# Kernel optimization log

Hardware: AMD Instinct MI355X
Metric: run time of the kernel (lower is better)

Reference implementation:

```python
import jax, jax.numpy as jnp
import numpy as np

B, S = 4, 1024
D = 256          # token_dim = channel_dim = expert_dim
D_LF = 768       # longformer hidden size
ADAPT = 128
NEXP = 4
HID = 64
DSUM = 3 * D + D_LF  # combiner concat width = 1536


def _gelu(v):
    return jax.nn.gelu(v, approximate=False)  # torch nn.GELU default = exact


def setup_inputs() -> dict:
    key = jax.random.key(0)
    ks = iter(jax.random.split(key, 40))
    def w(shape, scale=1.0):
        return jax.random.normal(next(ks), shape, jnp.float32) * scale
    z = lambda *shape: jnp.zeros(shape, jnp.float32)
    return dict(
        x=w((B, S, D)),
        lf_out=w((B, S, D_LF)),
        W_feat=w((D, ADAPT), D ** -0.5), b_feat=z(ADAPT),
        Wt=w((D, D), D ** -0.5), bt=z(D),
        Wt_a=w((ADAPT, D * D), 0.01 * ADAPT ** -0.5), bt_a=z(D * D),
        Wc=w((D, D), D ** -0.5), bc=z(D),
        Wc_a=w((ADAPT, D * D), 0.01 * ADAPT ** -0.5), bc_a=z(D * D),
        We=w((NEXP, D, D), D ** -0.5), be=z(NEXP, D),
        We_a=w((NEXP, ADAPT, D * D), 0.01 * ADAPT ** -0.5), be_a=z(NEXP, D * D),
        Wg=w((ADAPT, NEXP + 1), ADAPT ** -0.5), bg=z(NEXP + 1),
        Wphi=w((D, HID)), bphi=z(D, HID),
        Wpsi1=w((D * HID, HID), (D * HID) ** -0.5), bpsi1=z(HID),
        Wpsi2=w((HID, D), HID ** -0.5), bpsi2=z(D),
        Wres=w((DSUM, DSUM), DSUM ** -0.5), bres=z(DSUM),
        W1=w((DSUM, HID), DSUM ** -0.5), b1=z(HID),
        W2=w((HID, 4), HID ** -0.5), b2=z(4),
        Wo=w((DSUM, D), DSUM ** -0.5), bo=z(D),
    )


def reference(x, lf_out, W_feat, b_feat, Wt, bt, Wt_a, bt_a, Wc, bc, Wc_a, bc_a,
              We, be, We_a, be_a, Wg, bg, Wphi, bphi, Wpsi1, bpsi1, Wpsi2, bpsi2,
              Wres, bres, W1, b1, W2, b2, Wo, bo):
    Bx, Sx, d = x.shape
    N = Bx * Sx
    xf = x.reshape(N, d)
    lff = lf_out.reshape(N, -1)
    # featurizer -> per-token adapt features; global mean drives adaptive weights
    adapt = xf @ W_feat + b_feat            # [N, ADAPT]
    am = adapt.mean(axis=0)                 # [ADAPT] single adapt vector (LiquidLinear view constraint)

    def liquid(inp, Wb, bb, Wa, ba):
        Wdyn = Wb + (am @ Wa + ba).reshape(Wb.shape)
        return inp @ Wdyn + bb

    tok = liquid(xf, Wt, bt, Wt_a, bt_a)    # [N, D] token mixer
    chan = liquid(xf, Wc, bc, Wc_a, bc_a)   # [N, D] channel mixer

    # MixtureOfExperts: softmax gate over NEXP liquid experts + 1 KA expert
    gate = jax.nn.softmax(adapt @ Wg + bg, axis=-1)              # [N, NEXP+1]
    dW = (jnp.einsum('a,eaf->ef', am, We_a) + be_a).reshape(We.shape)
    eo = jnp.einsum('nd,edo->neo', xf, We + dW) + be[None]       # [N, E, D]
    # Kolmogorov-Arnold expert: per-feature phi (Linear(1,HID)+gelu), then psi MLP
    phi = _gelu(xf[:, :, None] * Wphi[None] + bphi[None])        # [N, D, HID]
    ka = _gelu(phi.reshape(N, -1) @ Wpsi1 + bpsi1) @ Wpsi2 + bpsi2
    moe = jnp.einsum('ne,ned->nd', gate[:, :-1], eo) + gate[:, -1:] * ka

    # ComponentCombination: learned softmax component weights + residual path
    concat = jnp.concatenate([tok, chan, moe, lff], axis=-1)     # [N, DSUM]
    residual = concat @ Wres + bres
    h = _gelu(concat @ W1 + b1)
    cw = jax.nn.softmax(h @ W2 + b2, axis=-1)                    # [N, 4]
    combined = jnp.concatenate(
        [cw[:, 0:1] * tok, cw[:, 1:2] * chan, cw[:, 2:3] * moe, cw[:, 3:4] * lff],
        axis=-1) + residual                                      # [N, DSUM]
    return (combined @ Wo + bo).reshape(Bx, Sx, d)
```

## Files before the change

### kernel.cpp

```cpp
#include <hip/hip_runtime.h>
#include <hip/hip_bf16.h>


__device__ __forceinline__ float gelu_f(float v){ return 0.5f*v*(1.0f + erff(v*0.70710678118654752f)); }

__device__ __forceinline__ float u16tof(unsigned short u){
  union { unsigned int i; float f; } v; v.i = ((unsigned int)u) << 16; return v.f;
}
__device__ __forceinline__ unsigned short f2b(float f){
  union { float f; unsigned int u; } v; v.f = f;
  unsigned int r = v.u + 0x7fffu + ((v.u >> 16) & 1u);
  return (unsigned short)(r >> 16);
}

using short8  = __attribute__((ext_vector_type(8))) short;
using float4v = __attribute__((ext_vector_type(4))) float;

template<int MODE>
__global__ __launch_bounds__(256) void mgemm_k(
    const unsigned short* __restrict__ A, const unsigned short* __restrict__ Bt,
    const float* __restrict__ bias, float* __restrict__ C,
    int M, int N, int K, long sB, long sBias, long sC)
{
  if constexpr (MODE==1){
    Bt   += sB   * blockIdx.z;
    bias += sBias* blockIdx.z;
    C    += sC   * blockIdx.z;
  }
  __shared__ __align__(16) unsigned short As[128][40];
  __shared__ __align__(16) unsigned short Bs[128][40];
  const int tid  = threadIdx.x;
  const int m0   = blockIdx.y*128, n0 = blockIdx.x*128;
  const int wave = tid>>6, lane = tid&63;
  const int wm   = (wave&1)*64, wn = (wave>>1)*64;
  const int q    = lane>>4, r = lane&15;
  const int sm   = tid>>2, sq = (tid&3)*8;

  float4v acc[4][4];
  #pragma unroll
  for (int i=0;i<4;i++)
    #pragma unroll
    for (int j=0;j<4;j++) acc[i][j] = (float4v){0.f,0.f,0.f,0.f};

  const unsigned short* Ap = A + (long)(m0+sm)*K + sq;
  const unsigned short* Bp = Bt + (long)(n0+sm)*K + sq;
  const long rstep = (long)64*K;

  for (int k0 = 0; k0 < K; k0 += 32){
    uint4 a0 = *(const uint4*)(Ap + k0);
    uint4 a1 = *(const uint4*)(Ap + k0 + rstep);
    uint4 b0 = *(const uint4*)(Bp + k0);
    uint4 b1 = *(const uint4*)(Bp + k0 + rstep);
    __syncthreads();
    *(uint4*)&As[sm   ][sq] = a0;
    *(uint4*)&As[sm+64][sq] = a1;
    *(uint4*)&Bs[sm   ][sq] = b0;
    *(uint4*)&Bs[sm+64][sq] = b1;
    __syncthreads();
    short8 af[4], bf[4];
    #pragma unroll
    for (int mt=0;mt<4;mt++) af[mt] = *(const short8*)&As[wm + mt*16 + r][q*8];
    #pragma unroll
    for (int nt=0;nt<4;nt++) bf[nt] = *(const short8*)&Bs[wn + nt*16 + r][q*8];
    #pragma unroll
    for (int mt=0;mt<4;mt++)
      #pragma unroll
      for (int nt=0;nt<4;nt++)
        acc[mt][nt] = __builtin_amdgcn_mfma_f32_16x16x32_bf16(af[mt], bf[nt], acc[mt][nt], 0, 0, 0);
  }

  #pragma unroll
  for (int nt=0;nt<4;nt++){
    int col = n0 + wn + nt*16 + r;
    float bb = bias[col];
    #pragma unroll
    for (int mt=0;mt<4;mt++){
      #pragma unroll
      for (int i=0;i<4;i++){
        int row = m0 + wm + mt*16 + q*4 + i;
        C[(long)row*N + col] = acc[mt][nt][i] + bb;
      }
    }
  }
}

__global__ __launch_bounds__(256) void psi1m_k(const float* __restrict__ x,
    const float* __restrict__ Wphi, const float* __restrict__ bphi,
    const unsigned short* __restrict__ Wpsi1_t, float* __restrict__ h1)
{
  __shared__ float xs[64][33];
  __shared__ __align__(16) unsigned int wbls[32][64];
  __shared__ __align__(16) unsigned short As[64][72];
  __shared__ __align__(16) unsigned short Bs[64][72];
  const int tid = threadIdx.x;
  const int m0 = blockIdx.x*64, d_lo = blockIdx.y*32;

  {
    int m = tid>>2, off = (tid&3)*8;
    const float* src = x + (long)(m0+m)*256 + d_lo + off;
    #pragma unroll
    for (int i=0;i<8;i++) xs[m][off+i] = src[i];
  }
  {
    #pragma unroll
    for (int i=0;i<2;i++){
      int idx4 = tid + 256*i;
      int rr = idx4>>4, cc = (idx4&15)*4;
      float4 w4 = *(const float4*)&Wphi[(long)(d_lo+rr)*64 + cc];
      float4 b4 = *(const float4*)&bphi[(long)(d_lo+rr)*64 + cc];
      uint4 p;
      p.x = (unsigned int)f2b(w4.x) | ((unsigned int)f2b(b4.x)<<16);
      p.y = (unsigned int)f2b(w4.y) | ((unsigned int)f2b(b4.y)<<16);
      p.z = (unsigned int)f2b(w4.z) | ((unsigned int)f2b(b4.z)<<16);
      p.w = (unsigned int)f2b(w4.w) | ((unsigned int)f2b(b4.w)<<16);
      *(uint4*)&wbls[rr][cc] = p;
    }
  }
  const int wave = tid>>6, lane = tid&63;
  const int wm = (wave&1)*32, wn = (wave>>1)*32;
  const int q = lane>>4, r = lane&15;
  const int pm = tid>>2, pk = (tid&3)*16;
  const int bn = tid>>2, bk = (tid&3)*16;

  float4v acc[2][2];
  #pragma unroll
  for (int i=0;i<2;i++)
    #pragma unroll
    for (int j=0;j<2;j++) acc[i][j] = (float4v){0.f,0.f,0.f,0.f};

  __syncthreads();

  for (int dd=0; dd<32; dd++){
    int dglob = d_lo + dd;
    const unsigned short* wp = Wpsi1_t + (long)bn*16384 + (long)dglob*64 + bk;
    uint4 b0 = *(const uint4*)wp;
    uint4 b1 = *(const uint4*)(wp + 8);
    float xv = xs[pm][dd];
    ushort4 ph[4];
    #pragma unroll
    for (int kk=0; kk<4; kk++){
      uint4 wb = *(const uint4*)&wbls[dd][pk + kk*4];
      unsigned int u[4] = {wb.x, wb.y, wb.z, wb.w};
      unsigned short o[4];
      #pragma unroll
      for (int e=0;e<4;e++){
        float w = u16tof((unsigned short)(u[e] & 0xffffu));
        float b = u16tof((unsigned short)(u[e] >> 16));
        o[e] = f2b(gelu_f(fmaf(xv, w, b)));
      }
      ph[kk].x=o[0]; ph[kk].y=o[1]; ph[kk].z=o[2]; ph[kk].w=o[3];
    }
    __syncthreads();
    *(uint4*)&Bs[bn][bk]   = b0;
    *(uint4*)&Bs[bn][bk+8] = b1;
    #pragma unroll
    for (int kk=0;kk<4;kk++) *(ushort4*)&As[pm][pk+kk*4] = ph[kk];
    __syncthreads();
    #pragma unroll
    for (int kb=0; kb<2; kb++){
      short8 af[2], bfr[2];
      #pragma unroll
      for (int mt=0;mt<2;mt++) af[mt]  = *(const short8*)&As[wm+mt*16+r][kb*32 + q*8];
      #pragma unroll
      for (int nt=0;nt<2;nt++) bfr[nt] = *(const short8*)&Bs[wn+nt*16+r][kb*32 + q*8];
      #pragma unroll
      for (int mt=0;mt<2;mt++)
        #pragma unroll
        for (int nt=0;nt<2;nt++)
          acc[mt][nt] = __builtin_amdgcn_mfma_f32_16x16x32_bf16(af[mt], bfr[nt], acc[mt][nt], 0, 0, 0);
    }
  }
  #pragma unroll
  for (int nt=0;nt<2;nt++){
    int col = wn + nt*16 + r;
    #pragma unroll
    for (int mt=0;mt<2;mt++)
      #pragma unroll
      for (int i=0;i<4;i++){
        int row = m0 + wm + mt*16 + q*4 + i;
        atomicAdd(&h1[(long)row*64 + col], acc[mt][nt][i]);
      }
  }
}

__global__ __launch_bounds__(256) void cvtb_k(const float* __restrict__ in, unsigned short* __restrict__ out){
  int i = (blockIdx.x*256 + threadIdx.x)*4;
  float4 v = *(const float4*)(in + i);
  ushort4 o; o.x = f2b(v.x); o.y = f2b(v.y); o.z = f2b(v.z); o.w = f2b(v.w);
  *(ushort4*)(out + i) = o;
}

__global__ __launch_bounds__(256) void tconv_k(const float* __restrict__ in, unsigned short* __restrict__ out, int R, int C){
  __shared__ float t[64][65];
  const int tid = threadIdx.x;
  const int c0 = blockIdx.x*64, r0 = blockIdx.y*64;
  const int lr = tid>>2, lc0 = (tid&3)*16;
  #pragma unroll
  for (int i=0;i<4;i++){
    float4 v = *(const float4*)&in[(long)(r0+lr)*C + c0 + lc0 + i*4];
    t[lr][lc0+i*4+0]=v.x; t[lr][lc0+i*4+1]=v.y; t[lr][lc0+i*4+2]=v.z; t[lr][lc0+i*4+3]=v.w;
  }
  __syncthreads();
  const int oc = tid>>2, os = (tid&3)*16;
  #pragma unroll
  for (int i=0;i<16;i++)
    out[(long)(c0+oc)*R + r0 + os + i] = f2b(t[os+i][oc]);
}

__device__ __forceinline__ float4 ld4(const float* p){ return *(const float4*)p; }
__device__ __forceinline__ float4 ld4(const unsigned short* p){
  ushort4 u = *(const ushort4*)p;
  return make_float4(u16tof(u.x), u16tof(u.y), u16tof(u.z), u16tof(u.w));
}
template<typename AT, int MODE>
__global__ __launch_bounds__(256) void gemm_k(
    const AT* __restrict__ A, const float* __restrict__ B, const float* __restrict__ bias,
    float* __restrict__ C, int M, int N, int K, int Kc)
{
  int klo = 0, khi = K;
  if constexpr (MODE==2){ klo = blockIdx.z*Kc; khi = klo + Kc; }
  __shared__ __align__(16) float As[16][68];
  __shared__ __align__(16) float Bs[16][68];
  const int tid = threadIdx.x;
  const int m0 = blockIdx.y*64, n0 = blockIdx.x*64;
  const int ty = tid>>4, tx = tid&15;
  const int ar = tid>>2, ac = (tid&3)*4;
  const int kr = tid>>4, nc = (tid&15)*4;
  float acc[4][4] = {};
  const AT* Ap = A + (long)(m0+ar)*K;

  for (int k0 = klo; k0 < khi; k0 += 16){
    float4 av = ld4(Ap + k0 + ac);
    float4 bv = *(const float4*)(B + (long)(k0+kr)*N + (n0+nc));
    __syncthreads();
    As[ac+0][ar] = av.x; As[ac+1][ar] = av.y; As[ac+2][ar] = av.z; As[ac+3][ar] = av.w;
    *(float4*)&Bs[kr][nc] = bv;
    __syncthreads();
    #pragma unroll
    for (int k = 0; k < 16; k++){
      float4 a4 = *(const float4*)&As[k][ty*4];
      float4 b4 = *(const float4*)&Bs[k][tx*4];
      float a[4] = {a4.x,a4.y,a4.z,a4.w};
      float b[4] = {b4.x,b4.y,b4.z,b4.w};
      #pragma unroll
      for (int i = 0; i < 4; i++)
        #pragma unroll
        for (int j = 0; j < 4; j++)
          acc[i][j] = fmaf(a[i], b[j], acc[i][j]);
    }
  }
  float bv4[4];
  #pragma unroll
  for (int j = 0; j < 4; j++) bv4[j] = bias[n0 + tx*4 + j];
  #pragma unroll
  for (int i = 0; i < 4; i++){
    long row = m0 + ty*4 + i;
    #pragma unroll
    for (int j = 0; j < 4; j++){
      float v = acc[i][j];
      if constexpr (MODE==2){
        if (blockIdx.z == 0) v += bv4[j];
        atomicAdd(&C[row*(long)N + n0 + tx*4 + j], v);
      } else {
        C[row*(long)N + n0 + tx*4 + j] = v + bv4[j];
      }
    }
  }
}

__global__ __launch_bounds__(256) void colmean_k(const float* __restrict__ adapt, float* __restrict__ am){
  __shared__ float red[256];
  int a = blockIdx.x, tid = threadIdx.x;
  float s = 0.f;
  for (int n = tid; n < 4096; n += 256) s += adapt[n*128 + a];
  red[tid] = s; __syncthreads();
  for (int w = 128; w > 0; w >>= 1){ if (tid < w) red[tid] += red[tid+w]; __syncthreads(); }
  if (tid == 0) am[a] = red[0] * (1.0f/4096.0f);
}

__global__ __launch_bounds__(256) void gate_k(const float* __restrict__ adapt,
    const float* __restrict__ Wg, const float* __restrict__ bg, float* __restrict__ gate){
  __shared__ float wg[640]; __shared__ float bgs[5];
  int tid = threadIdx.x;
  for (int i = tid; i < 640; i += 256) wg[i] = Wg[i];
  if (tid < 5) bgs[tid] = bg[tid];
  __syncthreads();
  int n = blockIdx.x*256 + tid;
  float l[5] = {bgs[0],bgs[1],bgs[2],bgs[3],bgs[4]};
  const float* ar = adapt + (long)n*128;
  for (int a = 0; a < 128; a++){
    float av = ar[a];
    #pragma unroll
    for (int e = 0; e < 5; e++) l[e] = fmaf(av, wg[a*5+e], l[e]);
  }
  float mx = l[0];
  #pragma unroll
  for (int e = 1; e < 5; e++) mx = fmaxf(mx, l[e]);
  float sum = 0.f;
  #pragma unroll
  for (int e = 0; e < 5; e++){ l[e] = expf(l[e]-mx); sum += l[e]; }
  float inv = 1.0f/sum;
  #pragma unroll
  for (int e = 0; e < 5; e++) gate[(long)n*5+e] = l[e]*inv;
}

__global__ __launch_bounds__(256) void dynw_k(const float* __restrict__ am,
    const float* Wt, const float* Wt_a, const float* bt_a,
    const float* Wc, const float* Wc_a, const float* bc_a,
    const float* We, const float* We_a, const float* be_a,
    unsigned short* __restrict__ Wdyn_t)
{
  __shared__ float ams[128];
  int tid = threadIdx.x;
  if (tid < 128) ams[tid] = am[tid];
  __syncthreads();
  long gid = (long)blockIdx.x*256 + tid;
  int seg = (int)(gid >> 16); int m = (int)(gid & 65535);
  const float *W, *Wa, *ba;
  if (seg == 0){ W = Wt; Wa = Wt_a; ba = bt_a; }
  else if (seg == 1){ W = Wc; Wa = Wc_a; ba = bc_a; }
  else { int e = seg-2; W = We + (long)e*65536; Wa = We_a + (long)e*65536*128; ba = be_a + (long)e*65536; }
  float s = W[m] + ba[m];
  for (int a = 0; a < 128; a++) s = fmaf(ams[a], Wa[(long)a*65536 + m], s);
  int row = m >> 8, col = m & 255;
  Wdyn_t[(long)seg*65536 + (long)col*256 + row] = f2b(s);
}

__global__ void bias6_k(const float* bt, const float* bc, const float* be, float* bias6){
  int z = blockIdx.x, t = threadIdx.x;
  const float* s = (z==0) ? bt : (z==1) ? bc : be + (long)(z-2)*256;
  bias6[z*256 + t] = s[t];
}

__global__ __launch_bounds__(256) void h1g_k(const float* __restrict__ h1,
    const float* __restrict__ bpsi1, float* __restrict__ h1g){
  int i = blockIdx.x*256 + threadIdx.x;
  h1g[i] = gelu_f(h1[i] + bpsi1[i & 63]);
}

__global__ __launch_bounds__(256) void concat_k(const float* __restrict__ tok,
    const float* __restrict__ chan, const float* __restrict__ eo,
    const float* __restrict__ gate, const float* __restrict__ ka,
    const float* __restrict__ lf, unsigned short* __restrict__ concat)
{
  int n = blockIdx.x, tid = threadIdx.x;
  const float* g = gate + (long)n*5;
  float g0=g[0], g1=g[1], g2=g[2], g3=g[3], g4=g[4];
  long nb = (long)n*1536;
  int d = tid;
  concat[nb + d]        = f2b(tok[(long)n*256 + d]);
  concat[nb + 256 + d]  = f2b(chan[(long)n*256 + d]);
  float m = g0*eo[(long)n*256 + d]
          + g1*eo[1048576 + (long)n*256 + d]
          + g2*eo[2097152 + (long)n*256 + d]
          + g3*eo[3145728 + (long)n*256 + d]
          + g4*ka[(long)n*256 + d];
  concat[nb + 512 + d] = f2b(m);
  for (int j = tid; j < 768; j += 256) concat[nb + 768 + j] = f2b(lf[(long)n*768 + j]);
}

__global__ __launch_bounds__(256) void cw_k(const float* __restrict__ hpre,
    const float* __restrict__ W2, const float* __restrict__ b2, float* __restrict__ cw){
  __shared__ float w2s[256]; __shared__ float b2s[4];
  int tid = threadIdx.x;
  w2s[tid] = W2[tid];
  if (tid < 4) b2s[tid] = b2[tid];
  __syncthreads();
  int n = blockIdx.x*256 + tid;
  float l[4] = {b2s[0],b2s[1],b2s[2],b2s[3]};
  const float* hp = hpre + (long)n*64;
  for (int j = 0; j < 64; j++){
    float hj = gelu_f(hp[j]);
    #pragma unroll
    for (int c = 0; c < 4; c++) l[c] = fmaf(hj, w2s[j*4+c], l[c]);
  }
  float mx = fmaxf(fmaxf(l[0],l[1]), fmaxf(l[2],l[3]));
  float sum = 0.f;
  #pragma unroll
  for (int c = 0; c < 4; c++){ l[c] = expf(l[c]-mx); sum += l[c]; }
  float inv = 1.0f/sum;
  #pragma unroll
  for (int c = 0; c < 4; c++) cw[(long)n*4+c] = l[c]*inv;
}

__global__ __launch_bounds__(256) void combine_k(unsigned short* __restrict__ concat,
    const float* __restrict__ residual, const float* __restrict__ cw){
  int n = blockIdx.x;
  int j = blockIdx.y*256 + threadIdx.x;
  int seg = (j < 768) ? (j >> 8) : 3;
  long idx = (long)n*1536 + j;
  float v = fmaf(cw[(long)n*4 + seg], u16tof(concat[idx]), residual[idx]);
  concat[idx] = f2b(v);
}

extern "C" void kernel_launch(void* const* d_in, const int* in_sizes, int n_in,
                              void* d_out, int out_size, void* d_ws, size_t ws_size,
                              hipStream_t stream)
{
  const float* x      = (const float*)d_in[0];
  const float* lf     = (const float*)d_in[1];
  const float* W_feat = (const float*)d_in[2];
  const float* b_feat = (const float*)d_in[3];
  const float* Wt     = (const float*)d_in[4];
  const float* bt     = (const float*)d_in[5];
  const float* Wt_a   = (const float*)d_in[6];
  const float* bt_a   = (const float*)d_in[7];
  const float* Wc     = (const float*)d_in[8];
  const float* bc     = (const float*)d_in[9];
  const float* Wc_a   = (const float*)d_in[10];
  const float* bc_a   = (const float*)d_in[11];
  const float* We     = (const float*)d_in[12];
  const float* be     = (const float*)d_in[13];
  const float* We_a   = (const float*)d_in[14];
  const float* be_a   = (const float*)d_in[15];
  const float* Wg     = (const float*)d_in[16];
  const float* bg     = (const float*)d_in[17];
  const float* Wphi   = (const float*)d_in[18];
  const float* bphi   = (const float*)d_in[19];
  const float* Wpsi1  = (const float*)d_in[20];
  const float* bpsi1  = (const float*)d_in[21];
  const float* Wpsi2  = (const float*)d_in[22];
  const float* bpsi2  = (const float*)d_in[23];
  const float* Wres   = (const float*)d_in[24];
  const float* bres   = (const float*)d_in[25];
  const float* W1     = (const float*)d_in[26];
  const float* b1     = (const float*)d_in[27];
  const float* W2     = (const float*)d_in[28];
  const float* b2     = (const float*)d_in[29];
  const float* Wo     = (const float*)d_in[30];
  const float* bo     = (const float*)d_in[31];

  float* ws = (float*)d_ws;
  float* T      = ws;
  float* tok    = T;
  float* chan   = T + 1048576;
  float* eo     = T + 2*1048576;
  float* adapt  = T + 6*1048576;
  float* am     = adapt + 524288;
  float* gate   = am + 128;
  float* bias6  = gate + 20480;
  float* h1     = bias6 + 1536;
  float* h1g    = h1 + 262144;
  float* ka     = h1g + 262144;
  unsigned short* xb      = (unsigned short*)(ka + 1048576);
  unsigned short* Wdyn_t  = xb + 1048576;
  unsigned short* Wres_t  = Wdyn_t + 393216;
  unsigned short* Wo_t    = Wres_t + 2359296;
  unsigned short* Wpsi1_t = Wo_t + 393216;
  unsigned short* concat  = Wpsi1_t + 1048576;
  float* residual = T;
  float* hpre   = adapt;
  float* cw     = adapt + 262144;

  dim3 b256(256);

  cvtb_k<<<dim3(1024), b256, 0, stream>>>(x, xb);
  tconv_k<<<dim3(24,24), b256, 0, stream>>>(Wres, Wres_t, 1536, 1536);
  tconv_k<<<dim3(4,24),  b256, 0, stream>>>(Wo,   Wo_t,   1536, 256);
  tconv_k<<<dim3(1,256), b256, 0, stream>>>(Wpsi1, Wpsi1_t, 16384, 64);

  gemm_k<float,0><<<dim3(2,64,1), b256, 0, stream>>>(x, W_feat, b_feat, adapt, 4096,128,256, 0);

  colmean_k<<<dim3(128), b256, 0, stream>>>(adapt, am);
  gate_k<<<dim3(16), b256, 0, stream>>>(adapt, Wg, bg, gate);

  dynw_k<<<dim3(1536), b256, 0, stream>>>(am, Wt,Wt_a,bt_a, Wc,Wc_a,bc_a, We,We_a,be_a, Wdyn_t);
  bias6_k<<<dim3(6), b256, 0, stream>>>(bt, bc, be, bias6);

  mgemm_k<1><<<dim3(2,32,6), b256, 0, stream>>>(xb, Wdyn_t, bias6, T, 4096,256,256, 65536,256,1048576);

  hipMemsetAsync(h1, 0, 262144*sizeof(float), stream);
  psi1m_k<<<dim3(64,8), b256, 0, stream>>>(x, Wphi, bphi, Wpsi1_t, h1);
  h1g_k<<<dim3(1024), b256, 0, stream>>>(h1, bpsi1, h1g);
  gemm_k<float,0><<<dim3(4,64,1), b256, 0, stream>>>(h1g, Wpsi2, bpsi2, ka, 4096,256,64, 0);

  concat_k<<<dim3(4096), b256, 0, stream>>>(tok, chan, eo, gate, ka, lf, concat);

  mgemm_k<0><<<dim3(12,32,1), b256, 0, stream>>>(concat, Wres_t, bres, residual, 4096,1536,1536, 0,0,0);

  hipMemsetAsync(hpre, 0, 262144*sizeof(float), stream);
  gemm_k<unsigned short,2><<<dim3(1,64,8), b256, 0, stream>>>(concat, W1, b1, hpre, 4096,64,1536, 192);
  cw_k<<<dim3(16), b256, 0, stream>>>(hpre, W2, b2, cw);

  combine_k<<<dim3(4096,6), b256, 0, stream>>>(concat, residual, cw);

  mgemm_k<0><<<dim3(2,32,1), b256, 0, stream>>>(concat, Wo_t, bo, (float*)d_out, 4096,256,1536, 0,0,0);
}
```

Measured before the change: 627.0 us.

## Fuse pipeline stages, split-K final GEMM, faster GELU and vectorized dynamic weights

Reworks most of the launch pipeline. The prep conversions merge into one kernel, and the column mean is folded into the adapt GEMM through atomics. The liquid, MoE and concat stages fuse into one MFMA kernel that writes bf16 concat directly, and GELU moves into the psi2 GEMM's A-load. The cw softmax joins combine, the W1 GEMM writes split-K partials without atomics, the output GEMM uses split-K with atomics, and dynw is vectorized by 4. The exact erf GELU is replaced by an Abramowitz-Stegun polynomial approximation. All of this cuts launches and intermediate fp32 traffic, at the cost of more atomics and slightly lower GELU accuracy.

```diff
diff --git a/kernel.cpp b/kernel.cpp
--- a/kernel.cpp
+++ b/kernel.cpp
@@ -1,8 +1,6 @@
 #include <hip/hip_runtime.h>
 #include <hip/hip_bf16.h>
 
-
-__device__ __forceinline__ float gelu_f(float v){ return 0.5f*v*(1.0f + erff(v*0.70710678118654752f)); }
 
 __device__ __forceinline__ float u16tof(unsigned short u){
   union { unsigned int i; float f; } v; v.i = ((unsigned int)u) << 16; return v.f;
@@ -13,6 +11,20 @@
   return (unsigned short)(r >> 16);
 }
 
+__device__ __forceinline__ float gelu_f(float v){
+  float y = fabsf(v) * 0.70710678118654752f;
+  float t = __builtin_amdgcn_rcpf(fmaf(0.3275911f, y, 1.0f));
+  float p = fmaf(1.061405429f, t, -1.453152027f);
+  p = fmaf(p, t, 1.421413741f);
+  p = fmaf(p, t, -0.284496736f);
+  p = fmaf(p, t, 0.254829592f);
+  p = p * t;
+  float e = __expf(-y*y);
+  float erf_y = fmaf(-p, e, 1.0f);
+  float s = copysignf(erf_y, v);
+  return 0.5f * v * (1.0f + s);
+}
+
 using short8  = __attribute__((ext_vector_type(8))) short;
 using float4v = __attribute__((ext_vector_type(4))) float;
 
@@ -20,13 +32,10 @@
 __global__ __launch_bounds__(256) void mgemm_k(
     const unsigned short* __restrict__ A, const unsigned short* __restrict__ Bt,
     const float* __restrict__ bias, float* __restrict__ C,
-    int M, int N, int K, long sB, long sBias, long sC)
-{
-  if constexpr (MODE==1){
-    Bt   += sB   * blockIdx.z;
-    bias += sBias* blockIdx.z;
-    C    += sC   * blockIdx.z;
-  }
+    int M, int N, int K, int Kc)
+{
+  int klo = 0, khi = K;
+  if constexpr (MODE==2){ klo = blockIdx.z*Kc; khi = klo + Kc; }
   __shared__ __align__(16) unsigned short As[128][40];
   __shared__ __align__(16) unsigned short Bs[128][40];
   const int tid  = threadIdx.x;
@@ -46,7 +55,7 @@
   const unsigned short* Bp = Bt + (long)(n0+sm)*K + sq;
   const long rstep = (long)64*K;
 
-  for (int k0 = 0; k0 < K; k0 += 32){
+  for (int k0 = klo; k0 < khi; k0 += 32){
     uint4 a0 = *(const uint4*)(Ap + k0);
     uint4 a1 = *(const uint4*)(Ap + k0 + rstep);
     uint4 b0 = *(const uint4*)(Bp + k0);
@@ -78,9 +87,121 @@
       #pragma unroll
       for (int i=0;i<4;i++){
         int row = m0 + wm + mt*16 + q*4 + i;
-        C[(long)row*N + col] = acc[mt][nt][i] + bb;
+        if constexpr (MODE==2){
+          float v = acc[mt][nt][i];
+          if (blockIdx.z == 0) v += bb;
+          atomicAdd(&C[(long)row*N + col], v);
+        } else {
+          C[(long)row*N + col] = acc[mt][nt][i] + bb;
+        }
       }
     }
+  }
+}
+
+__global__ __launch_bounds__(256) void liquid_k(
+    const unsigned short* __restrict__ xb, const unsigned short* __restrict__ Wdyn_t,
+    const float* __restrict__ bt, const float* __restrict__ bc, const float* __restrict__ be,
+    const float* __restrict__ gate, const float* __restrict__ ka, const float* __restrict__ lf,
+    unsigned short* __restrict__ concat)
+{
+  __shared__ __align__(16) unsigned short As[64][40];
+  __shared__ __align__(16) unsigned short Bs[64][40];
+  const int tid = threadIdx.x;
+  const int n0 = blockIdx.x*64, m0 = blockIdx.y*64;
+  const int wave = tid>>6, lane = tid&63;
+  const int wm = (wave&1)*32, wn = (wave>>1)*32;
+  const int q = lane>>4, r = lane&15;
+  const int sm = tid>>2, sq = (tid&3)*8;
+
+  {
+    int row = tid>>2, c0 = blockIdx.x*192 + (tid&3)*48;
+    const float* src = lf + (long)(m0+row)*768 + c0;
+    unsigned short* dst = concat + (long)(m0+row)*1536 + 768 + c0;
+    #pragma unroll
+    for (int i=0;i<12;i++){
+      float4 v = *(const float4*)(src + i*4);
+      ushort4 o; o.x=f2b(v.x); o.y=f2b(v.y); o.z=f2b(v.z); o.w=f2b(v.w);
+      *(ushort4*)(dst + i*4) = o;
+    }
+  }
+
+  float4v moe[2][2];
+  #pragma unroll
+  for (int i=0;i<2;i++)
+    #pragma unroll
+    for (int j=0;j<2;j++) moe[i][j] = (float4v){0.f,0.f,0.f,0.f};
+
+  const unsigned short* Ap = xb + (long)(m0+sm)*256 + sq;
+
+  for (int z=0; z<6; z++){
+    const unsigned short* Bp = Wdyn_t + (long)z*65536 + (long)(n0+sm)*256 + sq;
+    float4v acc[2][2];
+    #pragma unroll
+    for (int i=0;i<2;i++)
+      #pragma unroll
+      for (int j=0;j<2;j++) acc[i][j] = (float4v){0.f,0.f,0.f,0.f};
+    for (int k0=0; k0<256; k0+=32){
+      uint4 a0 = *(const uint4*)(Ap + k0);
+      uint4 b0 = *(const uint4*)(Bp + k0);
+      __syncthreads();
+      *(uint4*)&As[sm][sq] = a0;
+      *(uint4*)&Bs[sm][sq] = b0;
+      __syncthreads();
+      short8 af[2], bf[2];
+      #pragma unroll
+      for (int mt=0;mt<2;mt++) af[mt] = *(const short8*)&As[wm+mt*16+r][q*8];
+      #pragma unroll
+      for (int nt=0;nt<2;nt++) bf[nt] = *(const short8*)&Bs[wn+nt*16+r][q*8];
+      #pragma unroll
+      for (int mt=0;mt<2;mt++)
+        #pragma unroll
+        for (int nt=0;nt<2;nt++)
+          acc[mt][nt] = __builtin_amdgcn_mfma_f32_16x16x32_bf16(af[mt], bf[nt], acc[mt][nt], 0, 0, 0);
+    }
+    if (z < 2){
+      const float* bsrc = z ? bc : bt;
+      #pragma unroll
+      for (int nt=0;nt<2;nt++){
+        int col = n0 + wn + nt*16 + r;
+        float bb = bsrc[col];
+        #pragma unroll
+        for (int mt=0;mt<2;mt++)
+          #pragma unroll
+          for (int i=0;i<4;i++){
+            int row = m0 + wm + mt*16 + q*4 + i;
+            concat[(long)row*1536 + z*256 + col] = f2b(acc[mt][nt][i] + bb);
+          }
+      }
+    } else {
+      int e = z-2;
+      #pragma unroll
+      for (int nt=0;nt<2;nt++){
+        int col = n0 + wn + nt*16 + r;
+        float bb = be[e*256 + col];
+        #pragma unroll
+        for (int mt=0;mt<2;mt++)
+          #pragma unroll
+          for (int i=0;i<4;i++){
+            int row = m0 + wm + mt*16 + q*4 + i;
+            float g = gate[(long)row*5 + e];
+            moe[mt][nt][i] = fmaf(g, acc[mt][nt][i] + bb, moe[mt][nt][i]);
+          }
+      }
+    }
+  }
+  #pragma unroll
+  for (int nt=0;nt<2;nt++){
+    int col = n0 + wn + nt*16 + r;
+    #pragma unroll
+    for (int mt=0;mt<2;mt++)
+      #pragma unroll
+      for (int i=0;i<4;i++){
+        int row = m0 + wm + mt*16 + q*4 + i;
+        float g4 = gate[(long)row*5 + 4];
+        float v = fmaf(g4, ka[(long)row*256 + col], moe[mt][nt][i]);
+        concat[(long)row*1536 + 512 + col] = f2b(v);
+      }
   }
 }
 
@@ -88,33 +209,28 @@
     const float* __restrict__ Wphi, const float* __restrict__ bphi,
     const unsigned short* __restrict__ Wpsi1_t, float* __restrict__ h1)
 {
-  __shared__ float xs[64][33];
-  __shared__ __align__(16) unsigned int wbls[32][64];
+  __shared__ float xs[64][17];
+  __shared__ __align__(16) unsigned int wbls[16][64];
   __shared__ __align__(16) unsigned short As[64][72];
   __shared__ __align__(16) unsigned short Bs[64][72];
   const int tid = threadIdx.x;
-  const int m0 = blockIdx.x*64, d_lo = blockIdx.y*32;
+  const int m0 = blockIdx.x*64, d_lo = blockIdx.y*16;
 
   {
-    int m = tid>>2, off = (tid&3)*8;
-    const float* src = x + (long)(m0+m)*256 + d_lo + off;
-    #pragma unroll
-    for (int i=0;i<8;i++) xs[m][off+i] = src[i];
+    int m = tid>>2, off = (tid&3)*4;
+    float4 v = *(const float4*)(x + (long)(m0+m)*256 + d_lo + off);
+    xs[m][off+0]=v.x; xs[m][off+1]=v.y; xs[m][off+2]=v.z; xs[m][off+3]=v.w;
   }
   {
-    #pragma unroll
-    for (int i=0;i<2;i++){
-      int idx4 = tid + 256*i;
-      int rr = idx4>>4, cc = (idx4&15)*4;
-      float4 w4 = *(const float4*)&Wphi[(long)(d_lo+rr)*64 + cc];
-      float4 b4 = *(const float4*)&bphi[(long)(d_lo+rr)*64 + cc];
-      uint4 p;
-      p.x = (unsigned int)f2b(w4.x) | ((unsigned int)f2b(b4.x)<<16);
-      p.y = (unsigned int)f2b(w4.y) | ((unsigned int)f2b(b4.y)<<16);
-      p.z = (unsigned int)f2b(w4.z) | ((unsigned int)f2b(b4.z)<<16);
-      p.w = (unsigned int)f2b(w4.w) | ((unsigned int)f2b(b4.w)<<16);
-      *(uint4*)&wbls[rr][cc] = p;
-    }
+    int rr = tid>>4, cc = (tid&15)*4;
+    float4 w4 = *(const float4*)&Wphi[(long)(d_lo+rr)*64 + cc];
+    float4 b4 = *(const float4*)&bphi[(long)(d_lo+rr)*64 + cc];
+    uint4 p;
+    p.x = (unsigned int)f2b(w4.x) | ((unsigned int)f2b(b4.x)<<16);
+    p.y = (unsigned int)f2b(w4.y) | ((unsigned int)f2b(b4.y)<<16);
+    p.z = (unsigned int)f2b(w4.z) | ((unsigned int)f2b(b4.z)<<16);
+    p.w = (unsigned int)f2b(w4.w) | ((unsigned int)f2b(b4.w)<<16);
+    *(uint4*)&wbls[rr][cc] = p;
   }
   const int wave = tid>>6, lane = tid&63;
   const int wm = (wave&1)*32, wn = (wave>>1)*32;
@@ -130,7 +246,7 @@
 
   __syncthreads();
 
-  for (int dd=0; dd<32; dd++){
+  for (int dd=0; dd<16; dd++){
     int dglob = d_lo + dd;
     const unsigned short* wp = Wpsi1_t + (long)bn*16384 + (long)dglob*64 + bk;
     uint4 b0 = *(const uint4*)wp;
@@ -183,17 +299,26 @@
   }
 }
 
-__global__ __launch_bounds__(256) void cvtb_k(const float* __restrict__ in, unsigned short* __restrict__ out){
-  int i = (blockIdx.x*256 + threadIdx.x)*4;
-  float4 v = *(const float4*)(in + i);
-  ushort4 o; o.x = f2b(v.x); o.y = f2b(v.y); o.z = f2b(v.z); o.w = f2b(v.w);
-  *(ushort4*)(out + i) = o;
-}
-
-__global__ __launch_bounds__(256) void tconv_k(const float* __restrict__ in, unsigned short* __restrict__ out, int R, int C){
+__global__ __launch_bounds__(256) void prep_k(
+    const float* __restrict__ x, unsigned short* __restrict__ xb,
+    const float* __restrict__ Wres, unsigned short* __restrict__ Wres_t,
+    const float* __restrict__ Wo, unsigned short* __restrict__ Wo_t,
+    const float* __restrict__ Wpsi1, unsigned short* __restrict__ Wpsi1_t)
+{
   __shared__ float t[64][65];
-  const int tid = threadIdx.x;
-  const int c0 = blockIdx.x*64, r0 = blockIdx.y*64;
+  const int bid = blockIdx.x, tid = threadIdx.x;
+  if (bid < 1024){
+    int i = (bid*256 + tid)*4;
+    float4 v = *(const float4*)(x + i);
+    ushort4 o; o.x=f2b(v.x); o.y=f2b(v.y); o.z=f2b(v.z); o.w=f2b(v.w);
+    *(ushort4*)(xb + i) = o;
+    return;
+  }
+  const float* in; unsigned short* out; int R, C, bx, by;
+  if (bid < 1600){ int tt=bid-1024; bx=tt%24; by=tt/24; in=Wres;  out=Wres_t;  R=1536;  C=1536; }
+  else if (bid < 1696){ int tt=bid-1600; bx=tt%4; by=tt/4; in=Wo; out=Wo_t;    R=1536;  C=256; }
+  else { int tt=bid-1696; bx=0; by=tt; in=Wpsi1; out=Wpsi1_t; R=16384; C=64; }
+  const int c0 = bx*64, r0 = by*64;
   const int lr = tid>>2, lc0 = (tid&3)*16;
   #pragma unroll
   for (int i=0;i<4;i++){
@@ -212,13 +337,14 @@
   ushort4 u = *(const ushort4*)p;
   return make_float4(u16tof(u.x), u16tof(u.y), u16tof(u.z), u16tof(u.w));
 }
-template<typename AT, int MODE>
+template<typename AT, int MODE, int AGELU>
 __global__ __launch_bounds__(256) void gemm_k(
     const AT* __restrict__ A, const float* __restrict__ B, const float* __restrict__ bias,
-    float* __restrict__ C, int M, int N, int K, int Kc)
+    const float* __restrict__ abias, float* __restrict__ C,
+    int M, int N, int K, int Kc, long sC)
 {
   int klo = 0, khi = K;
-  if constexpr (MODE==2){ klo = blockIdx.z*Kc; khi = klo + Kc; }
+  if constexpr (MODE==3){ klo = blockIdx.z*Kc; khi = klo + Kc; C += sC*blockIdx.z; }
   __shared__ __align__(16) float As[16][68];
   __shared__ __align__(16) float Bs[16][68];
   const int tid = threadIdx.x;
@@ -231,6 +357,11 @@
 
   for (int k0 = klo; k0 < khi; k0 += 16){
     float4 av = ld4(Ap + k0 + ac);
+    if constexpr (AGELU){
+      float4 ab = *(const float4*)(abias + k0 + ac);
+      av.x = gelu_f(av.x + ab.x); av.y = gelu_f(av.y + ab.y);
+      av.z = gelu_f(av.z + ab.z); av.w = gelu_f(av.w + ab.w);
+    }
     float4 bv = *(const float4*)(B + (long)(k0+kr)*N + (n0+nc));
     __syncthreads();
     As[ac+0][ar] = av.x; As[ac+1][ar] = av.y; As[ac+2][ar] = av.z; As[ac+3][ar] = av.w;
@@ -249,33 +380,66 @@
           acc[i][j] = fmaf(a[i], b[j], acc[i][j]);
     }
   }
-  float bv4[4];
-  #pragma unroll
-  for (int j = 0; j < 4; j++) bv4[j] = bias[n0 + tx*4 + j];
+  float bv4[4] = {0.f,0.f,0.f,0.f};
+  if constexpr (MODE!=3){
+    #pragma unroll
+    for (int j = 0; j < 4; j++) bv4[j] = bias[n0 + tx*4 + j];
+  }
   #pragma unroll
   for (int i = 0; i < 4; i++){
     long row = m0 + ty*4 + i;
     #pragma unroll
-    for (int j = 0; j < 4; j++){
-      float v = acc[i][j];
-      if constexpr (MODE==2){
-        if (blockIdx.z == 0) v += bv4[j];
-        atomicAdd(&C[row*(long)N + n0 + tx*4 + j], v);
-      } else {
-        C[row*(long)N + n0 + tx*4 + j] = v + bv4[j];
-      }
-    }
-  }
-}
-
-__global__ __launch_bounds__(256) void colmean_k(const float* __restrict__ adapt, float* __restrict__ am){
-  __shared__ float red[256];
-  int a = blockIdx.x, tid = threadIdx.x;
-  float s = 0.f;
-  for (int n = tid; n < 4096; n += 256) s += adapt[n*128 + a];
-  red[tid] = s; __syncthreads();
-  for (int w = 128; w > 0; w >>= 1){ if (tid < w) red[tid] += red[tid+w]; __syncthreads(); }
-  if (tid == 0) am[a] = red[0] * (1.0f/4096.0f);
+    for (int j = 0; j < 4; j++)
+      C[row*(long)N + n0 + tx*4 + j] = acc[i][j] + bv4[j];
+  }
+}
+
+__global__ __launch_bounds__(256) void adapt_k(const float* __restrict__ A, const float* __restrict__ B,
+    const float* __restrict__ bias, float* __restrict__ C, float* __restrict__ amraw)
+{
+  const int K = 256, N = 128;
+  __shared__ __align__(16) float As[16][68];
+  __shared__ __align__(16) float Bs[16][68];
+  const int tid = threadIdx.x;
+  const int m0 = blockIdx.y*64, n0 = blockIdx.x*64;
+  const int ty = tid>>4, tx = tid&15;
+  const int ar = tid>>2, ac = (tid&3)*4;
+  const int kr = tid>>4, nc = (tid&15)*4;
+  float acc[4][4] = {};
+  const float* Ap = A + (long)(m0+ar)*K;
+  for (int k0 = 0; k0 < K; k0 += 16){
+    float4 av = *(const float4*)(Ap + k0 + ac);
+    float4 bv = *(const float4*)(B + (long)(k0+kr)*N + (n0+nc));
+    __syncthreads();
+    As[ac+0][ar] = av.x; As[ac+1][ar] = av.y; As[ac+2][ar] = av.z; As[ac+3][ar] = av.w;
+    *(float4*)&Bs[kr][nc] = bv;
+    __syncthreads();
+    #pragma unroll
+    for (int k = 0; k < 16; k++){
+      float4 a4 = *(const float4*)&As[k][ty*4];
+      float4 b4 = *(const float4*)&Bs[k][tx*4];
+      float a[4] = {a4.x,a4.y,a4.z,a4.w};
+      float b[4] = {b4.x,b4.y,b4.z,b4.w};
+      #pragma unroll
+      for (int i = 0; i < 4; i++)
+        #pragma unroll
+        for (int j = 0; j < 4; j++)
+          acc[i][j] = fmaf(a[i], b[j], acc[i][j]);
+    }
+  }
+  float colsum[4] = {};
+  #pragma unroll
+  for (int j = 0; j < 4; j++){
+    float bb = bias[n0 + tx*4 + j];
+    #pragma unroll
+    for (int i = 0; i < 4; i++){
+      float v = acc[i][j] + bb;
+      C[(long)(m0 + ty*4 + i)*N + n0 + tx*4 + j] = v;
+      colsum[j] += v;
+    }
+  }
+  #pragma unroll
+  for (int j = 0; j < 4; j++) atomicAdd(&amraw[n0 + tx*4 + j], colsum[j]);
 }
 
 __global__ __launch_bounds__(256) void gate_k(const float* __restrict__ adapt,
@@ -312,85 +476,69 @@
 {
   __shared__ float ams[128];
   int tid = threadIdx.x;
-  if (tid < 128) ams[tid] = am[tid];
+  if (tid < 128) ams[tid] = am[tid] * (1.0f/4096.0f);
   __syncthreads();
-  long gid = (long)blockIdx.x*256 + tid;
-  int seg = (int)(gid >> 16); int m = (int)(gid & 65535);
+  long g4 = ((long)blockIdx.x*256 + tid)*4;
+  int seg = (int)(g4 >> 16); int m = (int)(g4 & 65535);
   const float *W, *Wa, *ba;
   if (seg == 0){ W = Wt; Wa = Wt_a; ba = bt_a; }
   else if (seg == 1){ W = Wc; Wa = Wc_a; ba = bc_a; }
   else { int e = seg-2; W = We + (long)e*65536; Wa = We_a + (long)e*65536*128; ba = be_a + (long)e*65536; }
-  float s = W[m] + ba[m];
-  for (int a = 0; a < 128; a++) s = fmaf(ams[a], Wa[(long)a*65536 + m], s);
+  float4 s = *(const float4*)&W[m];
+  float4 bb = *(const float4*)&ba[m];
+  s.x += bb.x; s.y += bb.y; s.z += bb.z; s.w += bb.w;
+  for (int a = 0; a < 128; a++){
+    float av = ams[a];
+    float4 wa = *(const float4*)&Wa[(long)a*65536 + m];
+    s.x = fmaf(av, wa.x, s.x); s.y = fmaf(av, wa.y, s.y);
+    s.z = fmaf(av, wa.z, s.z); s.w = fmaf(av, wa.w, s.w);
+  }
   int row = m >> 8, col = m & 255;
-  Wdyn_t[(long)seg*65536 + (long)col*256 + row] = f2b(s);
-}
-
-__global__ void bias6_k(const float* bt, const float* bc, const float* be, float* bias6){
-  int z = blockIdx.x, t = threadIdx.x;
-  const float* s = (z==0) ? bt : (z==1) ? bc : be + (long)(z-2)*256;
-  bias6[z*256 + t] = s[t];
-}
-
-__global__ __launch_bounds__(256) void h1g_k(const float* __restrict__ h1,
-    const float* __restrict__ bpsi1, float* __restrict__ h1g){
-  int i = blockIdx.x*256 + threadIdx.x;
-  h1g[i] = gelu_f(h1[i] + bpsi1[i & 63]);
-}
-
-__global__ __launch_bounds__(256) void concat_k(const float* __restrict__ tok,
-    const float* __restrict__ chan, const float* __restrict__ eo,
-    const float* __restrict__ gate, const float* __restrict__ ka,
-    const float* __restrict__ lf, unsigned short* __restrict__ concat)
-{
+  unsigned short* o = Wdyn_t + (long)seg*65536 + (long)col*256 + row;
+  o[0]   = f2b(s.x);
+  o[256] = f2b(s.y);
+  o[512] = f2b(s.z);
+  o[768] = f2b(s.w);
+}
+
+__global__ __launch_bounds__(256) void combine2_k(const float* __restrict__ hpre,
+    const float* __restrict__ b1, const float* __restrict__ W2, const float* __restrict__ b2,
+    const float* __restrict__ residual, unsigned short* __restrict__ concat)
+{
+  __shared__ float red[64][4];
+  __shared__ float lv[4];
+  __shared__ float cws[4];
   int n = blockIdx.x, tid = threadIdx.x;
-  const float* g = gate + (long)n*5;
-  float g0=g[0], g1=g[1], g2=g[2], g3=g[3], g4=g[4];
-  long nb = (long)n*1536;
-  int d = tid;
-  concat[nb + d]        = f2b(tok[(long)n*256 + d]);
-  concat[nb + 256 + d]  = f2b(chan[(long)n*256 + d]);
-  float m = g0*eo[(long)n*256 + d]
-          + g1*eo[1048576 + (long)n*256 + d]
-          + g2*eo[2097152 + (long)n*256 + d]
-          + g3*eo[3145728 + (long)n*256 + d]
-          + g4*ka[(long)n*256 + d];
-  concat[nb + 512 + d] = f2b(m);
-  for (int j = tid; j < 768; j += 256) concat[nb + 768 + j] = f2b(lf[(long)n*768 + j]);
-}
-
-__global__ __launch_bounds__(256) void cw_k(const float* __restrict__ hpre,
-    const float* __restrict__ W2, const float* __restrict__ b2, float* __restrict__ cw){
-  __shared__ float w2s[256]; __shared__ float b2s[4];
-  int tid = threadIdx.x;
-  w2s[tid] = W2[tid];
-  if (tid < 4) b2s[tid] = b2[tid];
+  if (tid < 64){
+    float s = b1[tid];
+    #pragma unroll
+    for (int z=0; z<8; z++) s += hpre[(long)z*262144 + (long)n*64 + tid];
+    float hj = gelu_f(s);
+    float4 w = *(const float4*)&W2[tid*4];
+    red[tid][0]=hj*w.x; red[tid][1]=hj*w.y; red[tid][2]=hj*w.z; red[tid][3]=hj*w.w;
+  }
   __syncthreads();
-  int n = blockIdx.x*256 + tid;
-  float l[4] = {b2s[0],b2s[1],b2s[2],b2s[3]};
-  const float* hp = hpre + (long)n*64;
-  for (int j = 0; j < 64; j++){
-    float hj = gelu_f(hp[j]);
-    #pragma unroll
-    for (int c = 0; c < 4; c++) l[c] = fmaf(hj, w2s[j*4+c], l[c]);
-  }
-  float mx = fmaxf(fmaxf(l[0],l[1]), fmaxf(l[2],l[3]));
-  float sum = 0.f;
-  #pragma unroll
-  for (int c = 0; c < 4; c++){ l[c] = expf(l[c]-mx); sum += l[c]; }
-  float inv = 1.0f/sum;
-  #pragma unroll
-  for (int c = 0; c < 4; c++) cw[(long)n*4+c] = l[c]*inv;
-}
-
-__global__ __launch_bounds__(256) void combine_k(unsigned short* __restrict__ concat,
-    const float* __restrict__ residual, const float* __restrict__ cw){
-  int n = blockIdx.x;
-  int j = blockIdx.y*256 + threadIdx.x;
-  int seg = (j < 768) ? (j >> 8) : 3;
-  long idx = (long)n*1536 + j;
-  float v = fmaf(cw[(long)n*4 + seg], u16tof(concat[idx]), residual[idx]);
-  concat[idx] = f2b(v);
+  if (tid < 4){
+    float l = b2[tid];
+    for (int j=0;j<64;j++) l += red[j][tid];
+    lv[tid] = l;
+  }
+  __syncthreads();
+  if (tid == 0){
+    float mx = fmaxf(fmaxf(lv[0],lv[1]), fmaxf(lv[2],lv[3]));
+    float e0=expf(lv[0]-mx), e1=expf(lv[1]-mx), e2=expf(lv[2]-mx), e3=expf(lv[3]-mx);
+    float inv = 1.0f/(e0+e1+e2+e3);
+    cws[0]=e0*inv; cws[1]=e1*inv; cws[2]=e2*inv; cws[3]=e3*inv;
+  }
+  __syncthreads();
+  #pragma unroll
+  for (int it=0; it<6; it++){
+    int j = tid + it*256;
+    int seg = (j < 768) ? (j >> 8) : 3;
+    long idx = (long)n*1536 + j;
+    float v = fmaf(cws[seg], u16tof(concat[idx]), residual[idx]);
+    concat[idx] = f2b(v);
+  }
 }
 
 extern "C" void kernel_launch(void* const* d_in, const int* in_sizes, int n_in,
@@ -431,58 +579,40 @@
   const float* bo     = (const float*)d_in[31];
 
   float* ws = (float*)d_ws;
-  float* T      = ws;
-  float* tok    = T;
-  float* chan   = T + 1048576;
-  float* eo     = T + 2*1048576;
-  float* adapt  = T + 6*1048576;
-  float* am     = adapt + 524288;
-  float* gate   = am + 128;
-  float* bias6  = gate + 20480;
-  float* h1     = bias6 + 1536;
-  float* h1g    = h1 + 262144;
-  float* ka     = h1g + 262144;
-  unsigned short* xb      = (unsigned short*)(ka + 1048576);
+  float* am       = ws;
+  float* h1       = ws + 128;
+  float* adapt    = ws + 262272;
+  float* gate     = adapt + 524288;
+  float* ka       = gate + 20480;
+  float* residual = ka + 1048576;
+  float* hpre     = residual + 6291456;
+  unsigned short* xb      = (unsigned short*)(hpre + 2097152);
   unsigned short* Wdyn_t  = xb + 1048576;
   unsigned short* Wres_t  = Wdyn_t + 393216;
   unsigned short* Wo_t    = Wres_t + 2359296;
   unsigned short* Wpsi1_t = Wo_t + 393216;
   unsigned short* concat  = Wpsi1_t + 1048576;
-  float* residual = T;
-  float* hpre   = adapt;
-  float* cw     = adapt + 262144;
 
   dim3 b256(256);
 
-  cvtb_k<<<dim3(1024), b256, 0, stream>>>(x, xb);
-  tconv_k<<<dim3(24,24), b256, 0, stream>>>(Wres, Wres_t, 1536, 1536);
-  tconv_k<<<dim3(4,24),  b256, 0, stream>>>(Wo,   Wo_t,   1536, 256);
-  tconv_k<<<dim3(1,256), b256, 0, stream>>>(Wpsi1, Wpsi1_t, 16384, 64);
-
-  gemm_k<float,0><<<dim3(2,64,1), b256, 0, stream>>>(x, W_feat, b_feat, adapt, 4096,128,256, 0);
-
-  colmean_k<<<dim3(128), b256, 0, stream>>>(adapt, am);
+  hipMemsetAsync(ws, 0, (128 + 262144)*sizeof(float), stream);
+  prep_k<<<dim3(1952), b256, 0, stream>>>(x, xb, Wres, Wres_t, Wo, Wo_t, Wpsi1, Wpsi1_t);
+
+  adapt_k<<<dim3(2,64), b256, 0, stream>>>(x, W_feat, b_feat, adapt, am);
   gate_k<<<dim3(16), b256, 0, stream>>>(adapt, Wg, bg, gate);
-
-  dynw_k<<<dim3(1536), b256, 0, stream>>>(am, Wt,Wt_a,bt_a, Wc,Wc_a,bc_a, We,We_a,be_a, Wdyn_t);
-  bias6_k<<<dim3(6), b256, 0, stream>>>(bt, bc, be, bias6);
-
-  mgemm_k<1><<<dim3(2,32,6), b256, 0, stream>>>(xb, Wdyn_t, bias6, T, 4096,256,256, 65536,256,1048576);
-
-  hipMemsetAsync(h1, 0, 262144*sizeof(float), stream);
-  psi1m_k<<<dim3(64,8), b256, 0, stream>>>(x, Wphi, bphi, Wpsi1_t, h1);
-  h1g_k<<<dim3(1024), b256, 0, stream>>>(h1, bpsi1, h1g);
-  gemm_k<float,0><<<dim3(4,64,1), b256, 0, stream>>>(h1g, Wpsi2, bpsi2, ka, 4096,256,64, 0);
-
-  concat_k<<<dim3(4096), b256, 0, stream>>>(tok, chan, eo, gate, ka, lf, concat);
-
-  mgemm_k<0><<<dim3(12,32,1), b256, 0, stream>>>(concat, Wres_t, bres, residual, 4096,1536,1536, 0,0,0);
-
-  hipMemsetAsync(hpre, 0, 262144*sizeof(float), stream);
-  gemm_k<unsigned short,2><<<dim3(1,64,8), b256, 0, stream>>>(concat, W1, b1, hpre, 4096,64,1536, 192);
-  cw_k<<<dim3(16), b256, 0, stream>>>(hpre, W2, b2, cw);
-
-  combine_k<<<dim3(4096,6), b256, 0, stream>>>(concat, residual, cw);
-
-  mgemm_k<0><<<dim3(2,32,1), b256, 0, stream>>>(concat, Wo_t, bo, (float*)d_out, 4096,256,1536, 0,0,0);
-}
+  dynw_k<<<dim3(384), b256, 0, stream>>>(am, Wt,Wt_a,bt_a, Wc,Wc_a,bc_a, We,We_a,be_a, Wdyn_t);
+
+  psi1m_k<<<dim3(64,16), b256, 0, stream>>>(x, Wphi, bphi, Wpsi1_t, h1);
+  gemm_k<float,0,1><<<dim3(4,64), b256, 0, stream>>>(h1, Wpsi2, bpsi2, bpsi1, ka, 4096,256,64, 0,0);
+
+  liquid_k<<<dim3(4,64), b256, 0, stream>>>(xb, Wdyn_t, bt, bc, be, gate, ka, lf, concat);
+
+  mgemm_k<0><<<dim3(12,32), b256, 0, stream>>>(concat, Wres_t, bres, residual, 4096,1536,1536, 0);
+
+  gemm_k<unsigned short,3,0><<<dim3(1,64,8), b256, 0, stream>>>(concat, W1, nullptr, nullptr, hpre, 4096,64,1536, 192, 262144);
+
+  combine2_k<<<dim3(4096), b256, 0, stream>>>(hpre, b1, W2, b2, residual, concat);
+
+  hipMemsetAsync(d_out, 0, (size_t)out_size*sizeof(float), stream);
+  mgemm_k<2><<<dim3(2,32,4), b256, 0, stream>>>(concat, Wo_t, bo, (float*)d_out, 4096,256,1536, 384);
+}
```

After: 632.1 us. About the same (+0.8%).
